# Performance work log

Hardware: AMD Instinct MI355X
Metric: run time of the kernel (lower is better)

Reference implementation:

```python
import jax, jax.numpy as jnp
import numpy as np
from jax import lax

N_QUBITS = 4
DIM = 1 << N_QUBITS  # 16-dim statevector
_idx = np.arange(DIM)
# RX on qubit q mixes amplitude i with i ^ bit(q): new[i] = c*old[i] - 1j*s*old[i^mask]
RX_PERMS = [(_idx ^ (1 << (N_QUBITS - 1 - q))) for q in range(N_QUBITS)]
# BasicEntanglerLayers CNOT ring: (0,1),(1,2),(2,3),(3,0). CNOT is a self-inverse basis permutation.
CNOT_PERMS = []
for qc in range(N_QUBITS):
    qt = (qc + 1) % N_QUBITS
    cb, tb = N_QUBITS - 1 - qc, N_QUBITS - 1 - qt
    CNOT_PERMS.append(_idx ^ (((_idx >> cb) & 1) << tb))
# PauliZ expval signs per wire over the 16 basis states: [4, 16]
Z_SIGNS = jnp.asarray(np.stack([1.0 - 2.0 * ((_idx >> (N_QUBITS - 1 - q)) & 1)
                                for q in range(N_QUBITS)]).astype(np.float32))


def _rx(flat, q, theta):
    # flat: [B, 16] complex64; theta: [B] (embedding angles) or scalar (layer weight)
    c = jnp.cos(theta * 0.5)
    s = jnp.sin(theta * 0.5)
    if jnp.ndim(theta) == 1:
        c, s = c[:, None], s[:, None]
    return c * flat - 1j * s * flat[:, RX_PERMS[q]]


def vqc(angles, weights):
    """AngleEmbedding(RX) + BasicEntanglerLayers(RX + CNOT ring) + <Z_w> per wire.
    angles: [B, 4], weights: [L, 4] -> [B, 4] expvals."""
    B = angles.shape[0]
    flat = jnp.zeros((B, DIM), jnp.complex64).at[:, 0].set(1.0)
    for q in range(N_QUBITS):
        flat = _rx(flat, q, angles[:, q])
    for l in range(weights.shape[0]):
        for q in range(N_QUBITS):
            flat = _rx(flat, q, weights[l, q])
        for perm in CNOT_PERMS:
            flat = flat[:, perm]
    probs = jnp.abs(flat) ** 2  # [B, 16] real
    return (probs @ Z_SIGNS.T).astype(angles.dtype)  # [B, 4]


def setup_inputs() -> dict:
    key = jax.random.key(0)
    ks = jax.random.split(key, 9)
    B, T, F, H, NQ, NL = 1024, 512, 32, 128, 4, 1
    concat = F + H
    # xavier_uniform with gain=0.5 for the two classical linears, zero bias
    lim_in = 0.5 * np.sqrt(6.0 / (concat + NQ))
    lim_out = 0.5 * np.sqrt(6.0 / (NQ + H))
    two_pi = 2.0 * np.pi
    return {
        "x": jax.random.normal(ks[0], (B, T, F), jnp.float32),
        "W_in": jax.random.uniform(ks[1], (NQ, concat), jnp.float32, -lim_in, lim_in),
        "b_in": jnp.zeros((NQ,), jnp.float32),
        "W_out": jax.random.uniform(ks[2], (H, NQ), jnp.float32, -lim_out, lim_out),
        "b_out": jnp.zeros((H,), jnp.float32),
        "w_forget": jax.random.uniform(ks[3], (NL, NQ), jnp.float32, 0.0, two_pi),
        "w_input": jax.random.uniform(ks[4], (NL, NQ), jnp.float32, 0.0, two_pi),
        "w_update": jax.random.uniform(ks[5], (NL, NQ), jnp.float32, 0.0, two_pi),
        "w_output": jax.random.uniform(ks[6], (NL, NQ), jnp.float32, 0.0, two_pi),
    }


def reference(x, W_in, b_in, W_out, b_out, w_forget, w_input, w_update, w_output):
    B, T, F = x.shape
    H = W_out.shape[0]
    h0 = jnp.zeros((B, H), x.dtype)
    c0 = jnp.zeros((B, H), x.dtype)

    def step(carry, x_t):
        h, c = carry
        v = jnp.concatenate([h, x_t], axis=1)            # [B, H+F]
        y = jnp.pi * jnp.tanh(v @ W_in.T + b_in)         # angles, [B, 4]
        def gate(wq):
            return vqc(y, wq) @ W_out.T + b_out          # shared clayer_out, [B, H]
        f = jax.nn.sigmoid(gate(w_forget))
        i = jax.nn.sigmoid(gate(w_input))
        g = jnp.tanh(gate(w_update))
        o = jax.nn.sigmoid(gate(w_output))
        c = f * c + i * g
        h = o * jnp.tanh(c)
        return (h, c), h

    (h_t, c_t), hs = lax.scan(step, (h0, c0), jnp.swapaxes(x, 0, 1))
    hidden_seq = jnp.swapaxes(hs, 0, 1)                  # [B, T, H]
    return hidden_seq, (h_t, c_t)
```

## Files before the change

### kernel.cpp

```cpp
#include <hip/hip_runtime.h>
#include <math.h>

constexpr int Bc = 1024;
constexpr int Tc = 512;
constexpr int Fc = 32;
constexpr int Hc = 128;

typedef float v2f __attribute__((ext_vector_type(2)));

template<int CTRL>
__device__ __forceinline__ float dpp_add_step(float x) {
  int yi = __builtin_amdgcn_update_dpp(0, __float_as_int(x), CTRL, 0xf, 0xf, false);
  return x + __int_as_float(yi);
}

__device__ __forceinline__ float rdl(float v, int l) {
  return __int_as_float(__builtin_amdgcn_readlane(__float_as_int(v), l));
}

__device__ __forceinline__ v2f fma2(v2f a, v2f b, v2f c) { return a * b + c; }

__device__ __forceinline__ v2f sigm2(v2f z) {
  v2f v = 0.5f * z;
  v2f u = v * v;
  v2f p = fma2(u, fma2(u, (v2f)(0.13333334f), (v2f)(-0.33333334f)), (v2f)(1.0f));
  return fma2((v2f)(0.5f), v * p, (v2f)(0.5f));
}
__device__ __forceinline__ v2f tanh2_p7(v2f z) {
  v2f u = z * z;
  v2f p = fma2(u, fma2(u, fma2(u, (v2f)(-0.05396825f), (v2f)(0.13333334f)),
                       (v2f)(-0.33333334f)), (v2f)(1.0f));
  return z * p;
}
__device__ __forceinline__ v2f tanh2_p11(v2f c) {
  v2f u = c * c;
  v2f p = fma2(u, fma2(u, fma2(u, fma2(u, fma2(u, (v2f)(-0.0088632358f), (v2f)(0.021869489f)),
                                       (v2f)(-0.053968254f)), (v2f)(0.13333334f)),
                       (v2f)(-0.33333334f)), (v2f)(1.0f));
  return c * p;
}
__device__ __forceinline__ float tanh_exp(float p) {
  float ex = __builtin_amdgcn_exp2f(p * 2.8853900817779268f);
  float r = __builtin_amdgcn_rcpf(ex + 1.0f);
  return fmaf(-2.0f, r, 1.0f);
}

__global__ __launch_bounds__(256) void prex_kernel(
    const float* __restrict__ x, const float* __restrict__ W_in,
    const float* __restrict__ b_in, float* __restrict__ pre) {
  __shared__ float4 Wl[4][8];
  const int tid = threadIdx.x;
  if (tid < 32) {
    int q = tid >> 3, k = tid & 7;
    Wl[q][k] = ((const float4*)(W_in + q * 160 + 128))[k];
  }
  __syncthreads();
  const int row = blockIdx.x * 256 + tid;
  const float4* xr = (const float4*)(x + (size_t)row * Fc);
  float a0 = b_in[0], a1 = b_in[1], a2 = b_in[2], a3 = b_in[3];
#pragma unroll
  for (int k = 0; k < 8; ++k) {
    float4 xv = xr[k];
    float4 w0 = Wl[0][k], w1 = Wl[1][k], w2 = Wl[2][k], w3 = Wl[3][k];
    a0 = fmaf(xv.x, w0.x, fmaf(xv.y, w0.y, fmaf(xv.z, w0.z, fmaf(xv.w, w0.w, a0))));
    a1 = fmaf(xv.x, w1.x, fmaf(xv.y, w1.y, fmaf(xv.z, w1.z, fmaf(xv.w, w1.w, a1))));
    a2 = fmaf(xv.x, w2.x, fmaf(xv.y, w2.y, fmaf(xv.z, w2.z, fmaf(xv.w, w2.w, a2))));
    a3 = fmaf(xv.x, w3.x, fmaf(xv.y, w3.y, fmaf(xv.z, w3.z, fmaf(xv.w, w3.w, a3))));
  }
  float4 o;
  o.x = a0; o.y = a1; o.z = a2; o.w = a3;
  ((float4*)pre)[row] = o;
}

__global__ __launch_bounds__(256, 1) void qlstm_kernel(
    const float* __restrict__ pre, const float* __restrict__ W_in,
    const float* __restrict__ W_out, const float* __restrict__ b_out,
    const float* __restrict__ w_f, const float* __restrict__ w_i,
    const float* __restrict__ w_u, const float* __restrict__ w_o,
    float* __restrict__ out) {
  const int tid = threadIdx.x;
  const int lane = tid & 63;
  const int wv = tid >> 6;
  const int b = blockIdx.x * 4 + wv;

  v2f wA0, wA1, wB0, wB1;
  wA0 = (v2f){W_in[0 * 160 + lane], W_in[1 * 160 + lane]};
  wA1 = (v2f){W_in[2 * 160 + lane], W_in[3 * 160 + lane]};
  wB0 = (v2f){W_in[0 * 160 + 64 + lane], W_in[1 * 160 + 64 + lane]};
  wB1 = (v2f){W_in[2 * 160 + 64 + lane], W_in[3 * 160 + 64 + lane]};

  const float4 wo0 = ((const float4*)W_out)[lane];
  const float4 wo1 = ((const float4*)W_out)[lane + 64];
  v2f wom0 = (v2f){wo0.x, wo1.x};
  v2f wom1 = (v2f){wo0.y, wo1.y};
  v2f wom2 = (v2f){wo0.z, wo1.z};
  v2f wom3 = (v2f){wo0.w, wo1.w};
  v2f bo = (v2f){b_out[lane], b_out[lane + 64]};

  const float* wg[4] = {w_f, w_i, w_u, w_o};
  v2f cwA[4], cwB[4], nsA[4], nsB[4];
#pragma unroll
  for (int g = 0; g < 4; ++g) {
    float w0 = wg[g][0], w1 = wg[g][1], w2 = wg[g][2], w3 = wg[g][3];
    cwA[g] = (v2f){cosf(w0), cosf(w1)};
    cwB[g] = (v2f){cosf(w2), cosf(w3)};
    nsA[g] = (v2f){-sinf(w0), -sinf(w1)};
    nsB[g] = (v2f){-sinf(w2), -sinf(w3)};
  }

  const float4* pref4 = (const float4*)(pre + (size_t)b * Tc * 4);
  float* hout = out + (size_t)b * Tc * Hc;

  v2f h = (v2f)(0.0f), c = (v2f)(0.0f);

  float4 cur = pref4[lane];

  for (int tc = 0; tc < Tc; tc += 64) {
    int nc = (tc + 64 < Tc) ? (tc + 64) : tc;
    float4 nxt = pref4[nc + lane];

    for (int s = 0; s < 64; ++s) {
      const int t = tc + s;
      v2f r01 = fma2((v2f)(h.y), wB0, (v2f)(h.x) * wA0);
      v2f r23 = fma2((v2f)(h.y), wB1, (v2f)(h.x) * wA1);
      float q0 = r01.x, q1 = r01.y, q2 = r23.x, q3 = r23.y;
      q0 = dpp_add_step<0x111>(q0); q1 = dpp_add_step<0x111>(q1); q2 = dpp_add_step<0x111>(q2); q3 = dpp_add_step<0x111>(q3);
      q0 = dpp_add_step<0x112>(q0); q1 = dpp_add_step<0x112>(q1); q2 = dpp_add_step<0x112>(q2); q3 = dpp_add_step<0x112>(q3);
      q0 = dpp_add_step<0x114>(q0); q1 = dpp_add_step<0x114>(q1); q2 = dpp_add_step<0x114>(q2); q3 = dpp_add_step<0x114>(q3);
      q0 = dpp_add_step<0x118>(q0); q1 = dpp_add_step<0x118>(q1); q2 = dpp_add_step<0x118>(q2); q3 = dpp_add_step<0x118>(q3);
      q0 = dpp_add_step<0x142>(q0); q1 = dpp_add_step<0x142>(q1); q2 = dpp_add_step<0x142>(q2); q3 = dpp_add_step<0x142>(q3);
      q0 = dpp_add_step<0x143>(q0); q1 = dpp_add_step<0x143>(q1); q2 = dpp_add_step<0x143>(q2); q3 = dpp_add_step<0x143>(q3);
      float s0 = rdl(q0, 63), s1 = rdl(q1, 63), s2 = rdl(q2, 63), s3 = rdl(q3, 63);

      float p0 = s0 + rdl(cur.x, s);
      float p1 = s1 + rdl(cur.y, s);
      float p2 = s2 + rdl(cur.z, s);
      float p3 = s3 + rdl(cur.w, s);

      float t0 = tanh_exp(p0), t1 = tanh_exp(p1), t2 = tanh_exp(p2), t3 = tanh_exp(p3);
      float sn0 = __builtin_amdgcn_sinf(t0 * 0.5f), cs0 = __builtin_amdgcn_cosf(t0 * 0.5f);
      float sn1 = __builtin_amdgcn_sinf(t1 * 0.5f), cs1 = __builtin_amdgcn_cosf(t1 * 0.5f);
      float sn2 = __builtin_amdgcn_sinf(t2 * 0.5f), cs2 = __builtin_amdgcn_cosf(t2 * 0.5f);
      float sn3 = __builtin_amdgcn_sinf(t3 * 0.5f), cs3 = __builtin_amdgcn_cosf(t3 * 0.5f);
      v2f csA = (v2f){cs0, cs1}, csB = (v2f){cs2, cs3};
      v2f snA = (v2f){sn0, sn1}, snB = (v2f){sn2, sn3};

      v2f z[4];
#pragma unroll
      for (int g = 0; g < 4; ++g) {
        v2f cq01 = fma2(snA, nsA[g], csA * cwA[g]);
        v2f cq23 = fma2(snB, nsB[g], csB * cwB[g]);
        float e1 = cq01.x * cq01.y;
        float t23 = cq23.x * cq23.y;
        float e0 = cq01.y * t23;
        float e2 = e1 * cq23.x;
        float e3 = e1 * t23;
        z[g] = fma2((v2f)(e0), wom0,
               fma2((v2f)(e1), wom1,
               fma2((v2f)(e2), wom2,
               fma2((v2f)(e3), wom3, bo))));
      }

      v2f fg = sigm2(z[0]);
      v2f ig = sigm2(z[1]);
      v2f gg = tanh2_p7(z[2]);
      v2f og = sigm2(z[3]);
      c = fma2(fg, c, ig * gg);
      h = og * tanh2_p11(c);

      hout[t * Hc + lane] = h.x;
      hout[t * Hc + lane + 64] = h.y;
    }
    cur = nxt;
  }

  float* hfin = out + (size_t)Bc * Tc * Hc;
  float* cfin = hfin + (size_t)Bc * Hc;
  hfin[b * Hc + lane] = h.x;
  hfin[b * Hc + lane + 64] = h.y;
  cfin[b * Hc + lane] = c.x;
  cfin[b * Hc + lane + 64] = c.y;
}

extern "C" void kernel_launch(void* const* d_in, const int* in_sizes, int n_in,
                              void* d_out, int out_size, void* d_ws, size_t ws_size,
                              hipStream_t stream) {
  const float* x    = (const float*)d_in[0];
  const float* W_in = (const float*)d_in[1];
  const float* b_in = (const float*)d_in[2];
  const float* W_out= (const float*)d_in[3];
  const float* b_out= (const float*)d_in[4];
  const float* w_f  = (const float*)d_in[5];
  const float* w_i  = (const float*)d_in[6];
  const float* w_u  = (const float*)d_in[7];
  const float* w_o  = (const float*)d_in[8];
  float* out = (float*)d_out;
  float* pre = (float*)d_ws;

  prex_kernel<<<(Bc * Tc) / 256, 256, 0, stream>>>(x, W_in, b_in, pre);
  qlstm_kernel<<<Bc / 4, 256, 0, stream>>>(pre, W_in, W_out, b_out,
                                           w_f, w_i, w_u, w_o, out);
}
```

Baseline: 499.1 us.

## Distribute quantum gate math across lanes with transpose-style reduction and LDS exchange

Replaces the four separate 64-lane DPP reductions plus readlanes with a combined butterfly reduction: lanes swap pairs with DPP, then reduce with row shifts, swizzle and bpermute, so one reduction produces all four angle sums. Each of 16 lanes then computes a single (gate, qubit) cos/sin product instead of every lane computing all 16 redundantly. The expectation values are exchanged through shared memory, and pre-activations are staged in LDS rather than read with readlane. This cuts transcendental and reduction work on the serial per-timestep path, but adds LDS round trips and write/read ordering within the wave. The sin is computed as a shifted cos of a scaled argument, which depends on the hardware cos taking its input in revolutions.

```diff
diff --git a/kernel.cpp b/kernel.cpp
--- a/kernel.cpp
+++ b/kernel.cpp
@@ -9,13 +9,18 @@
 typedef float v2f __attribute__((ext_vector_type(2)));
 
 template<int CTRL>
-__device__ __forceinline__ float dpp_add_step(float x) {
-  int yi = __builtin_amdgcn_update_dpp(0, __float_as_int(x), CTRL, 0xf, 0xf, false);
-  return x + __int_as_float(yi);
-}
-
-__device__ __forceinline__ float rdl(float v, int l) {
-  return __int_as_float(__builtin_amdgcn_readlane(__float_as_int(v), l));
+__device__ __forceinline__ float dppmov(float x) {
+  return __int_as_float(__builtin_amdgcn_update_dpp(0, __float_as_int(x), CTRL, 0xf, 0xf, false));
+}
+template<int CTRL>
+__device__ __forceinline__ float dpp_add(float x) { return x + dppmov<CTRL>(x); }
+
+template<int IMM>
+__device__ __forceinline__ float swz(float x) {
+  return __int_as_float(__builtin_amdgcn_ds_swizzle(__float_as_int(x), IMM));
+}
+__device__ __forceinline__ float bperm(int addr, float x) {
+  return __int_as_float(__builtin_amdgcn_ds_bpermute(addr, __float_as_int(x)));
 }
 
 __device__ __forceinline__ v2f fma2(v2f a, v2f b, v2f c) { return a * b + c; }
@@ -38,11 +43,6 @@
                                        (v2f)(-0.053968254f)), (v2f)(0.13333334f)),
                        (v2f)(-0.33333334f)), (v2f)(1.0f));
   return c * p;
-}
-__device__ __forceinline__ float tanh_exp(float p) {
-  float ex = __builtin_amdgcn_exp2f(p * 2.8853900817779268f);
-  float r = __builtin_amdgcn_rcpf(ex + 1.0f);
-  return fmaf(-2.0f, r, 1.0f);
 }
 
 __global__ __launch_bounds__(256) void prex_kernel(
@@ -82,12 +82,16 @@
   const int lane = tid & 63;
   const int wv = tid >> 6;
   const int b = blockIdx.x * 4 + wv;
-
-  v2f wA0, wA1, wB0, wB1;
-  wA0 = (v2f){W_in[0 * 160 + lane], W_in[1 * 160 + lane]};
-  wA1 = (v2f){W_in[2 * 160 + lane], W_in[3 * 160 + lane]};
-  wB0 = (v2f){W_in[0 * 160 + 64 + lane], W_in[1 * 160 + 64 + lane]};
-  wB1 = (v2f){W_in[2 * 160 + 64 + lane], W_in[3 * 160 + 64 + lane]};
+  const int q = lane & 3;
+  const int g = (lane >> 2) & 3;
+
+  __shared__ float4 preS[4][64];
+  __shared__ float4 eS4[4][4];
+
+  v2f wA0 = (v2f){W_in[0 * 160 + lane], W_in[1 * 160 + lane]};
+  v2f wA1 = (v2f){W_in[2 * 160 + lane], W_in[3 * 160 + lane]};
+  v2f wB0 = (v2f){W_in[0 * 160 + 64 + lane], W_in[1 * 160 + 64 + lane]};
+  v2f wB1 = (v2f){W_in[2 * 160 + 64 + lane], W_in[3 * 160 + 64 + lane]};
 
   const float4 wo0 = ((const float4*)W_out)[lane];
   const float4 wo1 = ((const float4*)W_out)[lane + 64];
@@ -97,74 +101,86 @@
   v2f wom3 = (v2f){wo0.w, wo1.w};
   v2f bo = (v2f){b_out[lane], b_out[lane + 64]};
 
-  const float* wg[4] = {w_f, w_i, w_u, w_o};
-  v2f cwA[4], cwB[4], nsA[4], nsB[4];
-#pragma unroll
-  for (int g = 0; g < 4; ++g) {
-    float w0 = wg[g][0], w1 = wg[g][1], w2 = wg[g][2], w3 = wg[g][3];
-    cwA[g] = (v2f){cosf(w0), cosf(w1)};
-    cwB[g] = (v2f){cosf(w2), cosf(w3)};
-    nsA[g] = (v2f){-sinf(w0), -sinf(w1)};
-    nsB[g] = (v2f){-sinf(w2), -sinf(w3)};
-  }
+  const float* wgp = (g == 0) ? w_f : (g == 1) ? w_i : (g == 2) ? w_u : w_o;
+  const float wgq = wgp[q];
+  const float k1 = -cosf(wgq);
+  const float k2 = -sinf(wgq);
+
+  const bool b0s = (lane & 1) != 0;
+  const bool b1s = (lane & 2) != 0;
+  const bool s1b = (q == 1);
+  const bool s2b = (q == 2);
+  const int mMap = (0x0312 >> (q * 4)) & 0xF;
+  float* eptr = (float*)&eS4[wv][0] + (g * 4 + mMap);
+  const int x32 = (lane ^ 32) << 2;
+  const float* pbase = (const float*)&preS[wv][0] + q;
 
   const float4* pref4 = (const float4*)(pre + (size_t)b * Tc * 4);
   float* hout = out + (size_t)b * Tc * Hc;
 
   v2f h = (v2f)(0.0f), c = (v2f)(0.0f);
-
   float4 cur = pref4[lane];
 
   for (int tc = 0; tc < Tc; tc += 64) {
+    preS[wv][lane] = cur;
     int nc = (tc + 64 < Tc) ? (tc + 64) : tc;
     float4 nxt = pref4[nc + lane];
 
+#pragma unroll 4
     for (int s = 0; s < 64; ++s) {
       const int t = tc + s;
+
       v2f r01 = fma2((v2f)(h.y), wB0, (v2f)(h.x) * wA0);
       v2f r23 = fma2((v2f)(h.y), wB1, (v2f)(h.x) * wA1);
-      float q0 = r01.x, q1 = r01.y, q2 = r23.x, q3 = r23.y;
-      q0 = dpp_add_step<0x111>(q0); q1 = dpp_add_step<0x111>(q1); q2 = dpp_add_step<0x111>(q2); q3 = dpp_add_step<0x111>(q3);
-      q0 = dpp_add_step<0x112>(q0); q1 = dpp_add_step<0x112>(q1); q2 = dpp_add_step<0x112>(q2); q3 = dpp_add_step<0x112>(q3);
-      q0 = dpp_add_step<0x114>(q0); q1 = dpp_add_step<0x114>(q1); q2 = dpp_add_step<0x114>(q2); q3 = dpp_add_step<0x114>(q3);
-      q0 = dpp_add_step<0x118>(q0); q1 = dpp_add_step<0x118>(q1); q2 = dpp_add_step<0x118>(q2); q3 = dpp_add_step<0x118>(q3);
-      q0 = dpp_add_step<0x142>(q0); q1 = dpp_add_step<0x142>(q1); q2 = dpp_add_step<0x142>(q2); q3 = dpp_add_step<0x142>(q3);
-      q0 = dpp_add_step<0x143>(q0); q1 = dpp_add_step<0x143>(q1); q2 = dpp_add_step<0x143>(q2); q3 = dpp_add_step<0x143>(q3);
-      float s0 = rdl(q0, 63), s1 = rdl(q1, 63), s2 = rdl(q2, 63), s3 = rdl(q3, 63);
-
-      float p0 = s0 + rdl(cur.x, s);
-      float p1 = s1 + rdl(cur.y, s);
-      float p2 = s2 + rdl(cur.z, s);
-      float p3 = s3 + rdl(cur.w, s);
-
-      float t0 = tanh_exp(p0), t1 = tanh_exp(p1), t2 = tanh_exp(p2), t3 = tanh_exp(p3);
-      float sn0 = __builtin_amdgcn_sinf(t0 * 0.5f), cs0 = __builtin_amdgcn_cosf(t0 * 0.5f);
-      float sn1 = __builtin_amdgcn_sinf(t1 * 0.5f), cs1 = __builtin_amdgcn_cosf(t1 * 0.5f);
-      float sn2 = __builtin_amdgcn_sinf(t2 * 0.5f), cs2 = __builtin_amdgcn_cosf(t2 * 0.5f);
-      float sn3 = __builtin_amdgcn_sinf(t3 * 0.5f), cs3 = __builtin_amdgcn_cosf(t3 * 0.5f);
-      v2f csA = (v2f){cs0, cs1}, csB = (v2f){cs2, cs3};
-      v2f snA = (v2f){sn0, sn1}, snB = (v2f){sn2, sn3};
-
-      v2f z[4];
-#pragma unroll
-      for (int g = 0; g < 4; ++g) {
-        v2f cq01 = fma2(snA, nsA[g], csA * cwA[g]);
-        v2f cq23 = fma2(snB, nsB[g], csB * cwB[g]);
-        float e1 = cq01.x * cq01.y;
-        float t23 = cq23.x * cq23.y;
-        float e0 = cq01.y * t23;
-        float e2 = e1 * cq23.x;
-        float e3 = e1 * t23;
-        z[g] = fma2((v2f)(e0), wom0,
-               fma2((v2f)(e1), wom1,
-               fma2((v2f)(e2), wom2,
-               fma2((v2f)(e3), wom3, bo))));
-      }
-
-      v2f fg = sigm2(z[0]);
-      v2f ig = sigm2(z[1]);
-      v2f gg = tanh2_p7(z[2]);
-      v2f og = sigm2(z[3]);
+
+      float t01 = b0s ? r01.y : r01.x;
+      float u01 = b0s ? r01.x : r01.y;
+      float s01 = t01 + dppmov<0xB1>(u01);
+      float t23 = b0s ? r23.y : r23.x;
+      float u23 = b0s ? r23.x : r23.y;
+      float s23 = t23 + dppmov<0xB1>(u23);
+      float v1 = b1s ? s23 : s01;
+      float v2_ = b1s ? s01 : s23;
+      float p = v1 + dppmov<0x4E>(v2_);
+      p = dpp_add<0x124>(p);
+      p = dpp_add<0x128>(p);
+      p += swz<0x401F>(p);
+      p += bperm(x32, p);
+      p += pbase[s * 4];
+
+      float E = __builtin_amdgcn_exp2f(p * 2.8853900817779268f);
+      float uu = __builtin_amdgcn_rcpf(E + 1.0f);
+      float C = __builtin_amdgcn_cosf(uu);
+      float S = __builtin_amdgcn_cosf(uu - 0.25f);
+      float cq = fmaf(C, k1, S * k2);
+
+      float cw1 = swz<0x041F>(cq);
+      float cw2 = swz<0x081F>(cq);
+      float cw3 = swz<0x0C1F>(cq);
+      float aa = cq * cw1;
+      float dd = aa * cw2;
+      float e3v = dd * cw3;
+      float w1v = s2b ? e3v : dd;
+      float w2v = s1b ? aa : w1v;
+      *eptr = w2v;
+
+      float4 ef = eS4[wv][0];
+      float4 ei = eS4[wv][1];
+      float4 eu = eS4[wv][2];
+      float4 eo = eS4[wv][3];
+      v2f zf = fma2((v2f)(ef.x), wom0, fma2((v2f)(ef.y), wom1,
+               fma2((v2f)(ef.z), wom2, fma2((v2f)(ef.w), wom3, bo))));
+      v2f zi = fma2((v2f)(ei.x), wom0, fma2((v2f)(ei.y), wom1,
+               fma2((v2f)(ei.z), wom2, fma2((v2f)(ei.w), wom3, bo))));
+      v2f zu = fma2((v2f)(eu.x), wom0, fma2((v2f)(eu.y), wom1,
+               fma2((v2f)(eu.z), wom2, fma2((v2f)(eu.w), wom3, bo))));
+      v2f zo = fma2((v2f)(eo.x), wom0, fma2((v2f)(eo.y), wom1,
+               fma2((v2f)(eo.z), wom2, fma2((v2f)(eo.w), wom3, bo))));
+
+      v2f fg = sigm2(zf);
+      v2f ig = sigm2(zi);
+      v2f gg = tanh2_p7(zu);
+      v2f og = sigm2(zo);
       c = fma2(fg, c, ig * gg);
       h = og * tanh2_p11(c);
 
```

New measurement: 484.0 us. -3.0%, faster.
